# Performance work log

Hardware: AMD Instinct MI355X
Metric: run time of the kernel (lower is better)

Reference implementation:

```python
import jax, jax.numpy as jnp
import numpy as np

B, T, V, H = 16, 128, 32000, 768
P = H // 2
NBOW = 64
PAD = 0
EPS = 0.05     # label smoothing
TAU = 0.07
W_CE, W_AL, W_BOW, W_DIV, W_VAR = 1.0, 0.5, 0.2, 0.1, 0.05
BOW_IDS = jnp.arange(NBOW, dtype=jnp.int32) * 500  # registered buffer bow_indices_tensor


def _ln(x, g, b):
    m = jnp.mean(x, axis=-1, keepdims=True)
    v = jnp.mean((x - m) ** 2, axis=-1, keepdims=True)
    return (x - m) / jnp.sqrt(v + 1e-5) * g + b


def _l2norm(x):
    return x / jnp.maximum(jnp.linalg.norm(x, axis=-1, keepdims=True), 1e-12)


def _proj(x, g, bn, W1, b1, W2, b2):
    h = _ln(x, g, bn)
    h = jax.nn.gelu(h @ W1 + b1, approximate=False)  # torch nn.GELU default = exact
    return h @ W2 + b2


def setup_inputs() -> dict:
    key = jax.random.key(0)
    ks = jax.random.split(key, 12)
    s = 0.02
    return {
        "logits": jax.random.normal(ks[0], (B, T, V), dtype=jnp.float32),
        "labels": jax.random.randint(ks[1], (B, T), 0, V, dtype=jnp.int32),
        "attention_mask": jnp.ones((B, T), dtype=jnp.int32),
        "encoder_features": jax.random.normal(ks[2], (B, H), dtype=jnp.float32),
        "decoder_hidden": jax.random.normal(ks[3], (B, T, H), dtype=jnp.float32),
        "ln_g_e": jnp.ones((H,), jnp.float32), "ln_b_e": jnp.zeros((H,), jnp.float32),
        "W1_e": jax.random.normal(ks[4], (H, P), jnp.float32) * s, "b1_e": jnp.zeros((P,), jnp.float32),
        "W2_e": jax.random.normal(ks[5], (P, P), jnp.float32) * s, "b2_e": jnp.zeros((P,), jnp.float32),
        "ln_g_t": jnp.ones((H,), jnp.float32), "ln_b_t": jnp.zeros((H,), jnp.float32),
        "W1_t": jax.random.normal(ks[6], (H, P), jnp.float32) * s, "b1_t": jnp.zeros((P,), jnp.float32),
        "W2_t": jax.random.normal(ks[7], (P, P), jnp.float32) * s, "b2_t": jnp.zeros((P,), jnp.float32),
        "W_bow": jax.random.normal(ks[8], (H, NBOW), jnp.float32) * s, "b_bow": jnp.zeros((NBOW,), jnp.float32),
    }


def _forward(logits, labels, attention_mask, encoder_features, decoder_hidden,
             ln_g_e, ln_b_e, W1_e, b1_e, W2_e, b2_e,
             ln_g_t, ln_b_t, W1_t, b1_t, W2_t, b2_t,
             W_bow, b_bow):
    # --- label-smoothed CE over valid (non-pad, non -100) tokens ---
    valid = (labels != PAD) & (labels != -100)                      # (B,T)
    lab = jnp.clip(labels, 0, V - 1)
    lp = jax.nn.log_softmax(logits, axis=-1)                        # (B,T,V)
    lp_lab = jnp.take_along_axis(lp, lab[..., None], axis=-1)[..., 0]
    tok_loss = -((1.0 - EPS) * lp_lab + (EPS / V) * lp.sum(-1))     # smooth target = (1-eps) at label + eps/V everywhere
    vf = valid.astype(jnp.float32)
    ce = (tok_loss * vf).sum() / jnp.maximum(vf.sum(), 1.0)

    # --- contrastive alignment (InfoNCE both ways) ---
    m = attention_mask[..., None].astype(jnp.float32)               # (B,T,1)
    pooled = (decoder_hidden * m).sum(1) / jnp.maximum(m.sum(1), 1.0)
    z_e = _l2norm(_proj(encoder_features, ln_g_e, ln_b_e, W1_e, b1_e, W2_e, b2_e))
    z_t = _l2norm(_proj(pooled, ln_g_t, ln_b_t, W1_t, b1_t, W2_t, b2_t))
    sim = (z_e @ z_t.T) / TAU                                       # (B,B)
    li = -jnp.diag(jax.nn.log_softmax(sim, axis=-1)).mean()
    lj = -jnp.diag(jax.nn.log_softmax(sim.T, axis=-1)).mean()
    align = 0.5 * (li + lj)

    # --- BoW BCE: target[b,i] = any valid token of row b equals bow id i ---
    match = (lab[:, :, None] == BOW_IDS[None, None, :]) & valid[:, :, None]
    bow_t = match.any(axis=1).astype(jnp.float32)                   # (B,NBOW)
    bl = encoder_features @ W_bow + b_bow
    bce = jnp.mean(jnp.maximum(bl, 0.0) - bl * bow_t + jnp.log1p(jnp.exp(-jnp.abs(bl))))

    # --- diversity: mean |off-diagonal cosine sim| of encoder features ---
    nf = _l2norm(encoder_features)
    sm = nf @ nf.T
    off = 1.0 - jnp.eye(B, dtype=jnp.float32)
    div = (jnp.abs(sm) * off).sum() / (B * B - B)

    # --- variance: mean exp(-var_dim) (torch.var uses ddof=1) ---
    fvar = jnp.var(encoder_features, axis=0, ddof=1)
    var_l = jnp.mean(jnp.exp(-fvar))

    return W_CE * ce + W_AL * align + W_BOW * bce + W_DIV * div + W_VAR * var_l


def reference(logits, labels, attention_mask, encoder_features, decoder_hidden,
              ln_g_e, ln_b_e, W1_e, b1_e, W2_e, b2_e,
              ln_g_t, ln_b_t, W1_t, b1_t, W2_t, b2_t,
              W_bow, b_bow):
    return _forward(logits, labels, attention_mask, encoder_features, decoder_hidden,
                    ln_g_e, ln_b_e, W1_e, b1_e, W2_e, b2_e,
                    ln_g_t, ln_b_t, W1_t, b1_t, W2_t, b2_t,
                    W_bow, b_bow)
```

## Files before the change

kernel.cpp:

```cpp
#include <hip/hip_runtime.h>
#include <math.h>

#define BB 16
#define TT 128
#define VV 32000
#define HH 768
#define PP 384
#define NBOWD 64
#define EPS_LS 0.05f
#define TAUC 0.07f
#define NCE (BB * TT)
#define SMALLB 101

typedef float fvec4 __attribute__((ext_vector_type(4)));

__device__ __forceinline__ float blockReduceSum256(float v, float* sh4) {
  int tid = threadIdx.x;
#pragma unroll
  for (int m = 32; m > 0; m >>= 1) v += __shfl_xor(v, m, 64);
  if ((tid & 63) == 0) sh4[tid >> 6] = v;
  __syncthreads();
  float r = (sh4[0] + sh4[1]) + (sh4[2] + sh4[3]);
  __syncthreads();
  return r;
}

#define CONS(v, sA, sB, sxv)                                  \
  do {                                                        \
    sxv += (v.x + v.y) + (v.z + v.w);                         \
    sA += __expf(v.x) + __expf(v.y);                          \
    sB += __expf(v.z) + __expf(v.w);                          \
  } while (0)

#define NTL(p) __builtin_nontemporal_load(p)

__global__ __launch_bounds__(256) void fused_main(
    const float* __restrict__ logits, const int* __restrict__ labels, const int* __restrict__ amask,
    const float* __restrict__ enc, const float* __restrict__ dh,
    const float* __restrict__ g_e, const float* __restrict__ be_, const float* __restrict__ W1e,
    const float* __restrict__ b1e, const float* __restrict__ W2e, const float* __restrict__ b2e,
    const float* __restrict__ g_t, const float* __restrict__ bt_, const float* __restrict__ W1t,
    const float* __restrict__ b1t, const float* __restrict__ W2t, const float* __restrict__ b2t,
    const float* __restrict__ W_bow, const float* __restrict__ b_bow,
    float* __restrict__ tok, float* __restrict__ vfs,
    float* __restrict__ ze, float* __restrict__ zt,
    float* __restrict__ bowp, float* __restrict__ divp, float* __restrict__ var_p) {
  __shared__ float smem[2304];
  int tid = threadIdx.x;
  int blk = blockIdx.x;

  if (blk >= SMALLB) {
    int row = blk - SMALLB;
    const float* x = logits + (size_t)row * VV;
    const fvec4* x4 = (const fvec4*)x;
    const fvec4* xr = x4 + tid;
    float s0 = 0.f, s1 = 0.f, s2 = 0.f, s3 = 0.f;
    float sxa = 0.f, sxb = 0.f;

    fvec4 a0 = NTL(xr + 0),    a1 = NTL(xr + 256),  a2 = NTL(xr + 512),  a3 = NTL(xr + 768);
    fvec4 a4 = NTL(xr + 1024), a5 = NTL(xr + 1280), a6 = NTL(xr + 1536), a7 = NTL(xr + 1792);
    fvec4 b0 = NTL(xr + 2048), b1 = NTL(xr + 2304), b2 = NTL(xr + 2560), b3 = NTL(xr + 2816);
    fvec4 b4 = NTL(xr + 3072), b5 = NTL(xr + 3328), b6 = NTL(xr + 3584), b7 = NTL(xr + 3840);

    CONS(a0, s0, s1, sxa); CONS(a1, s2, s3, sxb);
    CONS(a2, s0, s1, sxa); CONS(a3, s2, s3, sxb);
    CONS(a4, s0, s1, sxa); CONS(a5, s2, s3, sxb);
    CONS(a6, s0, s1, sxa); CONS(a7, s2, s3, sxb);

    a0 = NTL(xr + 4096); a1 = NTL(xr + 4352); a2 = NTL(xr + 4608); a3 = NTL(xr + 4864);
    a4 = NTL(xr + 5120); a5 = NTL(xr + 5376); a6 = NTL(xr + 5632); a7 = NTL(xr + 5888);

    CONS(b0, s0, s1, sxa); CONS(b1, s2, s3, sxb);
    CONS(b2, s0, s1, sxa); CONS(b3, s2, s3, sxb);
    CONS(b4, s0, s1, sxa); CONS(b5, s2, s3, sxb);
    CONS(b6, s0, s1, sxa); CONS(b7, s2, s3, sxb);

    b0 = NTL(xr + 6144); b1 = NTL(xr + 6400); b2 = NTL(xr + 6656); b3 = NTL(xr + 6912);
    b4 = NTL(xr + 7168); b5 = NTL(xr + 7424); b6 = NTL(xr + 7680);

    CONS(a0, s0, s1, sxa); CONS(a1, s2, s3, sxb);
    CONS(a2, s0, s1, sxa); CONS(a3, s2, s3, sxb);
    CONS(a4, s0, s1, sxa); CONS(a5, s2, s3, sxb);
    CONS(a6, s0, s1, sxa); CONS(a7, s2, s3, sxb);

    if (tid < 64) {
      fvec4 t0 = NTL(x4 + 7936 + tid);
      CONS(t0, s0, s1, sxa);
    }

    CONS(b0, s0, s1, sxa); CONS(b1, s2, s3, sxb);
    CONS(b2, s0, s1, sxa); CONS(b3, s2, s3, sxb);
    CONS(b4, s0, s1, sxa); CONS(b5, s2, s3, sxb);
    CONS(b6, s0, s1, sxa);

    float s = (s0 + s1) + (s2 + s3);
    float sx = sxa + sxb;

#pragma unroll
    for (int m = 32; m > 0; m >>= 1) {
      s += __shfl_xor(s, m, 64);
      sx += __shfl_xor(sx, m, 64);
    }
    if ((tid & 63) == 0) { int wv = tid >> 6; smem[wv] = s; smem[4 + wv] = sx; }
    __syncthreads();
    if (tid == 0) {
      float S = (smem[0] + smem[1]) + (smem[2] + smem[3]);
      float SX = (smem[4] + smem[5]) + (smem[6] + smem[7]);
      float L = logf(S);
      int lab = labels[row];
      bool valid = (lab != 0) && (lab != -100);
      int lc = lab < 0 ? 0 : (lab > VV - 1 ? VV - 1 : lab);
      float xl = x[lc];
      float lp_lab = xl - L;
      float lp_sum = SX - (float)VV * L;
      float tl = -((1.f - EPS_LS) * lp_lab + (EPS_LS / (float)VV) * lp_sum);
      tok[row] = valid ? tl : 0.f;
      vfs[row] = valid ? 1.f : 0.f;
    }
    return;
  }

  int sblk = blk;

  if (sblk < 32) {
    float* xs = smem;
    float* hs = smem + 768;
    float* red = smem + 1152;
    float* mf = smem + 1408;
    float* fA = smem + 1536;
    float* fB = smem + 1920;
    bool is_t = sblk >= BB;
    int b = sblk & (BB - 1);
    const float *g, *bb_, *W1, *b1, *W2, *b2;
    float* zout;
    if (is_t) { g = g_t; bb_ = bt_; W1 = W1t; b1 = b1t; W2 = W2t; b2 = b2t; zout = zt; }
    else      { g = g_e; bb_ = be_; W1 = W1e; b1 = b1e; W2 = W2e; b2 = b2e; zout = ze; }

    if (is_t) {
      float mval = (tid < TT) ? (float)amask[b * TT + tid] : 0.f;
      if (tid < TT) mf[tid] = mval;
      float den = fmaxf(blockReduceSum256(mval, red), 1.f);
      const fvec4* dh4 = (const fvec4*)(dh + (size_t)b * TT * HH);
      if (tid < 192) {
        fvec4 aa = {0.f, 0.f, 0.f, 0.f}, ab = {0.f, 0.f, 0.f, 0.f};
#pragma unroll 8
        for (int t = 0; t < TT; t += 2) {
          aa += mf[t] * dh4[t * 192 + tid];
          ab += mf[t + 1] * dh4[(t + 1) * 192 + tid];
        }
        ((fvec4*)xs)[tid] = (aa + ab) * (1.f / den);
      }
    } else {
      if (tid < 192) ((fvec4*)xs)[tid] = ((const fvec4*)(enc + (size_t)b * HH))[tid];
    }
    __syncthreads();

    float s1 = 0.f, s2 = 0.f;
    for (int k = tid; k < HH; k += 256) { float v = xs[k]; s1 += v; s2 += v * v; }
    s1 = blockReduceSum256(s1, red);
    s2 = blockReduceSum256(s2, red);
    float mean = s1 / (float)HH;
    float var = s2 / (float)HH - mean * mean;
    float rstd = rsqrtf(var + 1e-5f);
    for (int k = tid; k < HH; k += 256) xs[k] = (xs[k] - mean) * rstd * g[k] + bb_[k];
    __syncthreads();

    {
      const fvec4* W1v = (const fvec4*)W1;
      if (tid < 192) {
        int kh = (tid >= 96) ? 1 : 0;
        int j4 = tid - 96 * kh;
        const fvec4* Wp = W1v + (size_t)(384 * kh) * 96 + j4;
        const float* xk = xs + 384 * kh;
        fvec4 aa = {0.f, 0.f, 0.f, 0.f}, ab = {0.f, 0.f, 0.f, 0.f};
#pragma unroll 8
        for (int k = 0; k < 384; k += 2) {
          aa += xk[k] * Wp[(size_t)k * 96];
          ab += xk[k + 1] * Wp[(size_t)(k + 1) * 96];
        }
        fvec4 acc = aa + ab;
        if (kh) ((fvec4*)fB)[j4] = acc; else ((fvec4*)fA)[j4] = acc;
      }
      __syncthreads();
      for (int j = tid; j < PP; j += 256) {
        float a = b1[j] + fA[j] + fB[j];
        hs[j] = 0.5f * a * (1.f + erff(a * 0.70710678118654752440f));
      }
      __syncthreads();
    }

    {
      const fvec4* W2v = (const fvec4*)W2;
      if (tid < 192) {
        int kh = (tid >= 96) ? 1 : 0;
        int j4 = tid - 96 * kh;
        const fvec4* Wp = W2v + (size_t)(192 * kh) * 96 + j4;
        const float* hk = hs + 192 * kh;
        fvec4 aa = {0.f, 0.f, 0.f, 0.f}, ab = {0.f, 0.f, 0.f, 0.f};
#pragma unroll 8
        for (int k = 0; k < 192; k += 2) {
          aa += hk[k] * Wp[(size_t)k * 96];
          ab += hk[k + 1] * Wp[(size_t)(k + 1) * 96];
        }
        fvec4 acc = aa + ab;
        if (kh) ((fvec4*)fB)[j4] = acc; else ((fvec4*)fA)[j4] = acc;
      }
      __syncthreads();
      for (int j = tid; j < PP; j += 256) xs[j] = b2[j] + fA[j] + fB[j];
      __syncthreads();
    }

    float sq = 0.f;
    for (int j = tid; j < PP; j += 256) { float v = xs[j]; sq += v * v; }
    sq = blockReduceSum256(sq, red);
    float inv = 1.f / fmaxf(sqrtf(sq), 1e-12f);
    for (int j = tid; j < PP; j += 256) zout[b * PP + j] = xs[j] * inv;
    return;
  }

  if (sblk < 96) {
    int bb = sblk - 32;
    int b = bb >> 2, kq = bb & 3;
    int iw = tid & 63, ks = tid >> 6;
    const float* er = enc + b * HH;
    int k0 = kq * 192 + ks * 48;
    float acc = 0.f;
#pragma unroll 8
    for (int k = 0; k < 48; ++k) acc += er[k0 + k] * W_bow[(k0 + k) * NBOWD + iw];
    smem[ks * 64 + iw] = acc;
    __syncthreads();
    if (tid < 64) bowp[bb * 64 + tid] = smem[tid] + smem[64 + tid] + smem[128 + tid] + smem[192 + tid];
    return;
  }

  if (sblk < 100) {
    int kq = sblk - 96;
    int i = tid >> 4, j = tid & 15;
    const float* a = enc + i * HH + kq * 192;
    const float* c = enc + j * HH + kq * 192;
    float a0 = 0.f, a1 = 0.f;
#pragma unroll 8
    for (int k = 0; k < 192; k += 2) {
      a0 += a[k] * c[k];
      a1 += a[k + 1] * c[k + 1];
    }
    divp[kq * 256 + tid] = a0 + a1;
    return;
  }

  {
    float vsum = 0.f;
    for (int d = tid; d < HH; d += 256) {
      float a1 = 0.f, a2 = 0.f;
#pragma unroll
      for (int b = 0; b < BB; b++) { float v = enc[b * HH + d]; a1 += v; a2 += v * v; }
      float mean = a1 / (float)BB;
      float vr = (a2 - (float)BB * mean * mean) / (float)(BB - 1);
      vsum += __expf(-vr);
    }
    float r = blockReduceSum256(vsum, smem);
    if (tid == 0) var_p[0] = r / (float)HH;
  }
}

__global__ __launch_bounds__(256) void finalize2(
    const float* __restrict__ tok, const float* __restrict__ vfs,
    const float* __restrict__ ze, const float* __restrict__ zt,
    const float* __restrict__ bowp, const float* __restrict__ divp, const float* __restrict__ var_p,
    const int* __restrict__ labels, const float* __restrict__ b_bow,
    float* __restrict__ out) {
  __shared__ float sh[8];
  __shared__ float smat[256];
  __shared__ float misc[40];
  __shared__ int flags[BB * NBOWD];
  int tid = threadIdx.x;

  for (int i = tid; i < BB * NBOWD; i += 256) flags[i] = 0;
  __syncthreads();
  for (int i = tid; i < BB * TT; i += 256) {
    int lab = labels[i];
    if (lab != 0 && lab != -100) {
      int lc = lab < 0 ? 0 : (lab > VV - 1 ? VV - 1 : lab);
      if (lc % 500 == 0) {
        int iw = lc / 500;
        if (iw < NBOWD) flags[(i >> 7) * NBOWD + iw] = 1;
      }
    }
  }

  float tsum = 0.f, csum = 0.f;
  for (int i = tid; i < BB * TT; i += 256) { tsum += tok[i]; csum += vfs[i]; }
  float ce_sum = blockReduceSum256(tsum, sh);
  float ce_cnt = blockReduceSum256(csum, sh);

  {
    int i = tid >> 4, j = tid & 15;
    const float* a = ze + i * PP;
    const float* c = zt + j * PP;
    float a0 = 0.f, a1 = 0.f;
#pragma unroll 8
    for (int k = 0; k < PP; k += 2) { a0 += a[k] * c[k]; a1 += a[k + 1] * c[k + 1]; }
    smat[tid] = (a0 + a1) * (1.f / TAUC);
  }
  __syncthreads();
  if (tid < 32) {
    bool isrow = tid < 16;
    int r = tid & 15;
    float mx = -1e30f;
    for (int j = 0; j < 16; j++) { float v = isrow ? smat[r * 16 + j] : smat[j * 16 + r]; mx = fmaxf(mx, v); }
    float se = 0.f;
    for (int j = 0; j < 16; j++) { float v = isrow ? smat[r * 16 + j] : smat[j * 16 + r]; se += __expf(v - mx); }
    misc[tid] = smat[r * 17] - mx - logf(se);
  }
  __syncthreads();
  float align;
  if (tid == 0) {
    float li = 0.f, lj = 0.f;
    for (int r = 0; r < 16; r++) { li += misc[r]; lj += misc[16 + r]; }
    misc[33] = 0.5f * (-(li / 16.f) - (lj / 16.f));
  }
  __syncthreads();
  align = misc[33];
  __syncthreads();

  float bsum = 0.f;
  for (int e = tid; e < BB * NBOWD; e += 256) {
    int b = e >> 6, iw = e & 63;
    float bl = b_bow[iw] + bowp[(b * 4 + 0) * 64 + iw] + bowp[(b * 4 + 1) * 64 + iw]
             + bowp[(b * 4 + 2) * 64 + iw] + bowp[(b * 4 + 3) * 64 + iw];
    float tgt = (float)flags[e];
    bsum += fmaxf(bl, 0.f) - bl * tgt + log1pf(__expf(-fabsf(bl)));
  }
  float bce = blockReduceSum256(bsum, sh) / (float)(BB * NBOWD);

  smat[tid] = divp[tid] + divp[256 + tid] + divp[512 + tid] + divp[768 + tid];
  __syncthreads();
  float contrib = 0.f;
  {
    int i = tid >> 4, j = tid & 15;
    if (i != j) {
      float ni = fmaxf(sqrtf(smat[i * 17]), 1e-12f);
      float nj = fmaxf(sqrtf(smat[j * 17]), 1e-12f);
      contrib = fabsf(smat[tid]) / (ni * nj);
    }
  }
  float divs = blockReduceSum256(contrib, sh) / (float)(BB * BB - BB);

  if (tid == 0) {
    float ce = ce_sum / fmaxf(ce_cnt, 1.f);
    out[0] = 1.0f * ce + 0.5f * align + 0.2f * bce + 0.1f * divs + 0.05f * var_p[0];
  }
}

extern "C" void kernel_launch(void* const* d_in, const int* in_sizes, int n_in,
                              void* d_out, int out_size, void* d_ws, size_t ws_size,
                              hipStream_t stream) {
  const float* logits = (const float*)d_in[0];
  const int* labels   = (const int*)d_in[1];
  const int* amask    = (const int*)d_in[2];
  const float* enc    = (const float*)d_in[3];
  const float* dh     = (const float*)d_in[4];
  const float* g_e    = (const float*)d_in[5];
  const float* be_    = (const float*)d_in[6];
  const float* W1e    = (const float*)d_in[7];
  const float* b1e    = (const float*)d_in[8];
  const float* W2e    = (const float*)d_in[9];
  const float* b2e    = (const float*)d_in[10];
  const float* g_t    = (const float*)d_in[11];
  const float* bt_    = (const float*)d_in[12];
  const float* W1t    = (const float*)d_in[13];
  const float* b1t    = (const float*)d_in[14];
  const float* W2t    = (const float*)d_in[15];
  const float* b2t    = (const float*)d_in[16];
  const float* W_bow  = (const float*)d_in[17];
  const float* b_bow  = (const float*)d_in[18];

  float* f     = (float*)d_ws;
  float* tok   = f;
  float* vfs   = f + 2048;
  float* ze    = f + 4096;
  float* zt    = f + 10240;
  float* bowp  = f + 16384;
  float* divp  = f + 20480;
  float* var_p = f + 21504;

  fused_main<<<SMALLB + NCE, 256, 0, stream>>>(
      logits, labels, amask, enc, dh,
      g_e, be_, W1e, b1e, W2e, b2e,
      g_t, bt_, W1t, b1t, W2t, b2t,
      W_bow, b_bow, tok, vfs, ze, zt, bowp, divp, var_p);
  finalize2<<<1, 256, 0, stream>>>(tok, vfs, ze, zt, bowp, divp, var_p, labels, b_bow, (float*)d_out);
}
```

Before: 413.7 us.

## Split projection MLPs into batched kernels and parallelize decoder pooling

Before, 32 blocks each ran a full LayerNorm+MLP for a single sample, so every block re-read W1 and W2. Those blocks now only do masked mean pooling of decoder_hidden, spread over 96 blocks. The MLP moves into two separate kernels (mlp1, mlp2), each using 48 blocks over 16-column slices, which computes all 16 rows per block so weights are read once. L2 normalization is folded into finalize2. The cost is two extra kernel launches and serialization after the large CE pass, since the MLP can no longer overlap with the logits streaming.

```diff
diff --git a/kernel.cpp b/kernel.cpp
--- a/kernel.cpp
+++ b/kernel.cpp
@@ -10,7 +10,7 @@
 #define EPS_LS 0.05f
 #define TAUC 0.07f
 #define NCE (BB * TT)
-#define SMALLB 101
+#define SMALL1 165
 
 typedef float fvec4 __attribute__((ext_vector_type(4)));
 
@@ -34,23 +34,19 @@
 
 #define NTL(p) __builtin_nontemporal_load(p)
 
-__global__ __launch_bounds__(256) void fused_main(
+__global__ __launch_bounds__(256) void ce_pool(
     const float* __restrict__ logits, const int* __restrict__ labels, const int* __restrict__ amask,
     const float* __restrict__ enc, const float* __restrict__ dh,
-    const float* __restrict__ g_e, const float* __restrict__ be_, const float* __restrict__ W1e,
-    const float* __restrict__ b1e, const float* __restrict__ W2e, const float* __restrict__ b2e,
-    const float* __restrict__ g_t, const float* __restrict__ bt_, const float* __restrict__ W1t,
-    const float* __restrict__ b1t, const float* __restrict__ W2t, const float* __restrict__ b2t,
-    const float* __restrict__ W_bow, const float* __restrict__ b_bow,
+    const float* __restrict__ W_bow,
     float* __restrict__ tok, float* __restrict__ vfs,
-    float* __restrict__ ze, float* __restrict__ zt,
+    float* __restrict__ pooled,
     float* __restrict__ bowp, float* __restrict__ divp, float* __restrict__ var_p) {
-  __shared__ float smem[2304];
+  __shared__ float smem[1280];
   int tid = threadIdx.x;
   int blk = blockIdx.x;
 
-  if (blk >= SMALLB) {
-    int row = blk - SMALLB;
+  if (blk >= SMALL1) {
+    int row = blk - SMALL1;
     const float* x = logits + (size_t)row * VV;
     const fvec4* x4 = (const fvec4*)x;
     const fvec4* xr = x4 + tid;
@@ -120,106 +116,35 @@
     return;
   }
 
-  int sblk = blk;
-
-  if (sblk < 32) {
-    float* xs = smem;
-    float* hs = smem + 768;
-    float* red = smem + 1152;
-    float* mf = smem + 1408;
-    float* fA = smem + 1536;
-    float* fB = smem + 1920;
-    bool is_t = sblk >= BB;
-    int b = sblk & (BB - 1);
-    const float *g, *bb_, *W1, *b1, *W2, *b2;
-    float* zout;
-    if (is_t) { g = g_t; bb_ = bt_; W1 = W1t; b1 = b1t; W2 = W2t; b2 = b2t; zout = zt; }
-    else      { g = g_e; bb_ = be_; W1 = W1e; b1 = b1e; W2 = W2e; b2 = b2e; zout = ze; }
-
-    if (is_t) {
-      float mval = (tid < TT) ? (float)amask[b * TT + tid] : 0.f;
-      if (tid < TT) mf[tid] = mval;
-      float den = fmaxf(blockReduceSum256(mval, red), 1.f);
-      const fvec4* dh4 = (const fvec4*)(dh + (size_t)b * TT * HH);
-      if (tid < 192) {
-        fvec4 aa = {0.f, 0.f, 0.f, 0.f}, ab = {0.f, 0.f, 0.f, 0.f};
-#pragma unroll 8
-        for (int t = 0; t < TT; t += 2) {
-          aa += mf[t] * dh4[t * 192 + tid];
-          ab += mf[t + 1] * dh4[(t + 1) * 192 + tid];
-        }
-        ((fvec4*)xs)[tid] = (aa + ab) * (1.f / den);
-      }
-    } else {
-      if (tid < 192) ((fvec4*)xs)[tid] = ((const fvec4*)(enc + (size_t)b * HH))[tid];
-    }
+  if (blk < 96) {
+    float* mf = smem;
+    float* red = smem + 128;
+    fvec4* part = (fvec4*)(smem + 136);
+    int b = blk / 6, c = blk % 6;
+    float mval = (tid < TT) ? (float)amask[b * TT + tid] : 0.f;
+    if (tid < TT) mf[tid] = mval;
+    float den = fmaxf(blockReduceSum256(mval, red), 1.f);
+    int col = tid & 31, tg = tid >> 5;
+    const fvec4* dh4 = (const fvec4*)dh + (size_t)b * TT * 192 + c * 32 + col;
+    fvec4 acc = {0.f, 0.f, 0.f, 0.f};
+#pragma unroll 8
+    for (int i = 0; i < 16; ++i) {
+      int t = tg * 16 + i;
+      acc += mf[t] * dh4[(size_t)t * 192];
+    }
+    part[tg * 32 + col] = acc;
     __syncthreads();
-
-    float s1 = 0.f, s2 = 0.f;
-    for (int k = tid; k < HH; k += 256) { float v = xs[k]; s1 += v; s2 += v * v; }
-    s1 = blockReduceSum256(s1, red);
-    s2 = blockReduceSum256(s2, red);
-    float mean = s1 / (float)HH;
-    float var = s2 / (float)HH - mean * mean;
-    float rstd = rsqrtf(var + 1e-5f);
-    for (int k = tid; k < HH; k += 256) xs[k] = (xs[k] - mean) * rstd * g[k] + bb_[k];
-    __syncthreads();
-
-    {
-      const fvec4* W1v = (const fvec4*)W1;
-      if (tid < 192) {
-        int kh = (tid >= 96) ? 1 : 0;
-        int j4 = tid - 96 * kh;
-        const fvec4* Wp = W1v + (size_t)(384 * kh) * 96 + j4;
-        const float* xk = xs + 384 * kh;
-        fvec4 aa = {0.f, 0.f, 0.f, 0.f}, ab = {0.f, 0.f, 0.f, 0.f};
-#pragma unroll 8
-        for (int k = 0; k < 384; k += 2) {
-          aa += xk[k] * Wp[(size_t)k * 96];
-          ab += xk[k + 1] * Wp[(size_t)(k + 1) * 96];
-        }
-        fvec4 acc = aa + ab;
-        if (kh) ((fvec4*)fB)[j4] = acc; else ((fvec4*)fA)[j4] = acc;
-      }
-      __syncthreads();
-      for (int j = tid; j < PP; j += 256) {
-        float a = b1[j] + fA[j] + fB[j];
-        hs[j] = 0.5f * a * (1.f + erff(a * 0.70710678118654752440f));
-      }
-      __syncthreads();
-    }
-
-    {
-      const fvec4* W2v = (const fvec4*)W2;
-      if (tid < 192) {
-        int kh = (tid >= 96) ? 1 : 0;
-        int j4 = tid - 96 * kh;
-        const fvec4* Wp = W2v + (size_t)(192 * kh) * 96 + j4;
-        const float* hk = hs + 192 * kh;
-        fvec4 aa = {0.f, 0.f, 0.f, 0.f}, ab = {0.f, 0.f, 0.f, 0.f};
-#pragma unroll 8
-        for (int k = 0; k < 192; k += 2) {
-          aa += hk[k] * Wp[(size_t)k * 96];
-          ab += hk[k + 1] * Wp[(size_t)(k + 1) * 96];
-        }
-        fvec4 acc = aa + ab;
-        if (kh) ((fvec4*)fB)[j4] = acc; else ((fvec4*)fA)[j4] = acc;
-      }
-      __syncthreads();
-      for (int j = tid; j < PP; j += 256) xs[j] = b2[j] + fA[j] + fB[j];
-      __syncthreads();
-    }
-
-    float sq = 0.f;
-    for (int j = tid; j < PP; j += 256) { float v = xs[j]; sq += v * v; }
-    sq = blockReduceSum256(sq, red);
-    float inv = 1.f / fmaxf(sqrtf(sq), 1e-12f);
-    for (int j = tid; j < PP; j += 256) zout[b * PP + j] = xs[j] * inv;
+    if (tid < 32) {
+      fvec4 s = part[tid];
+#pragma unroll
+      for (int g2 = 1; g2 < 8; ++g2) s += part[g2 * 32 + tid];
+      ((fvec4*)pooled)[b * 192 + c * 32 + tid] = s * (1.f / den);
+    }
     return;
   }
 
-  if (sblk < 96) {
-    int bb = sblk - 32;
+  if (blk < 160) {
+    int bb = blk - 96;
     int b = bb >> 2, kq = bb & 3;
     int iw = tid & 63, ks = tid >> 6;
     const float* er = enc + b * HH;
@@ -233,8 +158,8 @@
     return;
   }
 
-  if (sblk < 100) {
-    int kq = sblk - 96;
+  if (blk < 164) {
+    int kq = blk - 160;
     int i = tid >> 4, j = tid & 15;
     const float* a = enc + i * HH + kq * 192;
     const float* c = enc + j * HH + kq * 192;
@@ -263,15 +188,100 @@
   }
 }
 
+__global__ __launch_bounds__(256) void mlp1(
+    const float* __restrict__ enc, const float* __restrict__ pooled,
+    const float* __restrict__ g_e, const float* __restrict__ be_, const float* __restrict__ W1e,
+    const float* __restrict__ b1e,
+    const float* __restrict__ g_t, const float* __restrict__ bt_, const float* __restrict__ W1t,
+    const float* __restrict__ b1t,
+    float* __restrict__ hmid) {
+  __shared__ float xsl[16 * 768];
+  int tid = threadIdx.x;
+  int side = blockIdx.x / 24, jc = blockIdx.x % 24;
+  int j0 = jc * 16;
+  const float* X = side ? pooled : enc;
+  const float* g = side ? g_t : g_e;
+  const float* bb_ = side ? bt_ : be_;
+  const float* W1 = side ? W1t : W1e;
+  const float* b1 = side ? b1t : b1e;
+
+  {
+    const fvec4* X4 = (const fvec4*)X;
+    fvec4* xs4 = (fvec4*)xsl;
+#pragma unroll
+    for (int i = 0; i < 12; ++i) xs4[tid + i * 256] = X4[tid + i * 256];
+  }
+  __syncthreads();
+
+  int r = tid >> 4, l = tid & 15;
+  float s1 = 0.f, s2 = 0.f;
+  for (int k = l; k < HH; k += 16) { float v = xsl[r * HH + k]; s1 += v; s2 += v * v; }
+#pragma unroll
+  for (int m = 8; m > 0; m >>= 1) { s1 += __shfl_xor(s1, m, 16); s2 += __shfl_xor(s2, m, 16); }
+  float mean = s1 / (float)HH;
+  float var = s2 / (float)HH - mean * mean;
+  float rstd = rsqrtf(var + 1e-5f);
+  for (int k = l; k < HH; k += 16) {
+    xsl[r * HH + k] = (xsl[r * HH + k] - mean) * rstd * g[k] + bb_[k];
+  }
+  __syncthreads();
+
+  int j = j0 + l;
+  const float* Wj = W1 + j;
+  const float* xr = xsl + r * HH;
+  float a0 = 0.f, a1 = 0.f;
+#pragma unroll 8
+  for (int k = 0; k < HH; k += 2) {
+    a0 += xr[k] * Wj[(size_t)k * PP];
+    a1 += xr[k + 1] * Wj[(size_t)(k + 1) * PP];
+  }
+  float acc = b1[j] + a0 + a1;
+  hmid[(side * 16 + r) * PP + j] = 0.5f * acc * (1.f + erff(acc * 0.70710678118654752440f));
+}
+
+__global__ __launch_bounds__(256) void mlp2(
+    const float* __restrict__ hmid,
+    const float* __restrict__ W2e, const float* __restrict__ b2e,
+    const float* __restrict__ W2t, const float* __restrict__ b2t,
+    float* __restrict__ zraw) {
+  __shared__ float hsl[16 * 384];
+  int tid = threadIdx.x;
+  int side = blockIdx.x / 24, jc = blockIdx.x % 24;
+  int j0 = jc * 16;
+  const float* W2 = side ? W2t : W2e;
+  const float* b2 = side ? b2t : b2e;
+
+  {
+    const fvec4* H4 = (const fvec4*)(hmid + side * 16 * PP);
+    fvec4* hs4 = (fvec4*)hsl;
+#pragma unroll
+    for (int i = 0; i < 6; ++i) hs4[tid + i * 256] = H4[tid + i * 256];
+  }
+  __syncthreads();
+
+  int r = tid >> 4, l = tid & 15;
+  int j = j0 + l;
+  const float* Wj = W2 + j;
+  const float* hr = hsl + r * PP;
+  float a0 = 0.f, a1 = 0.f;
+#pragma unroll 8
+  for (int k = 0; k < PP; k += 2) {
+    a0 += hr[k] * Wj[(size_t)k * PP];
+    a1 += hr[k + 1] * Wj[(size_t)(k + 1) * PP];
+  }
+  zraw[(side * 16 + r) * PP + j] = b2[j] + a0 + a1;
+}
+
 __global__ __launch_bounds__(256) void finalize2(
     const float* __restrict__ tok, const float* __restrict__ vfs,
-    const float* __restrict__ ze, const float* __restrict__ zt,
+    const float* __restrict__ zraw,
     const float* __restrict__ bowp, const float* __restrict__ divp, const float* __restrict__ var_p,
     const int* __restrict__ labels, const float* __restrict__ b_bow,
     float* __restrict__ out) {
   __shared__ float sh[8];
   __shared__ float smat[256];
   __shared__ float misc[40];
+  __shared__ float nrm[32];
   __shared__ int flags[BB * NBOWD];
   int tid = threadIdx.x;
 
@@ -294,13 +304,23 @@
   float ce_cnt = blockReduceSum256(csum, sh);
 
   {
+    int r = tid >> 3, l = tid & 7;
+    float sq = 0.f;
+    for (int k = l; k < PP; k += 8) { float v = zraw[r * PP + k]; sq += v * v; }
+#pragma unroll
+    for (int m = 4; m > 0; m >>= 1) sq += __shfl_xor(sq, m, 8);
+    if (l == 0) nrm[r] = fmaxf(sqrtf(sq), 1e-12f);
+  }
+  __syncthreads();
+
+  {
     int i = tid >> 4, j = tid & 15;
-    const float* a = ze + i * PP;
-    const float* c = zt + j * PP;
+    const float* a = zraw + i * PP;
+    const float* c = zraw + (16 + j) * PP;
     float a0 = 0.f, a1 = 0.f;
 #pragma unroll 8
     for (int k = 0; k < PP; k += 2) { a0 += a[k] * c[k]; a1 += a[k + 1] * c[k + 1]; }
-    smat[tid] = (a0 + a1) * (1.f / TAUC);
+    smat[tid] = (a0 + a1) / (nrm[i] * nrm[16 + j] * TAUC);
   }
   __syncthreads();
   if (tid < 32) {
@@ -375,19 +395,20 @@
   const float* W_bow  = (const float*)d_in[17];
   const float* b_bow  = (const float*)d_in[18];
 
-  float* f     = (float*)d_ws;
-  float* tok   = f;
-  float* vfs   = f + 2048;
-  float* ze    = f + 4096;
-  float* zt    = f + 10240;
-  float* bowp  = f + 16384;
-  float* divp  = f + 20480;
-  float* var_p = f + 21504;
-
-  fused_main<<<SMALLB + NCE, 256, 0, stream>>>(
-      logits, labels, amask, enc, dh,
-      g_e, be_, W1e, b1e, W2e, b2e,
-      g_t, bt_, W1t, b1t, W2t, b2t,
-      W_bow, b_bow, tok, vfs, ze, zt, bowp, divp, var_p);
-  finalize2<<<1, 256, 0, stream>>>(tok, vfs, ze, zt, bowp, divp, var_p, labels, b_bow, (float*)d_out);
-}
+  float* f      = (float*)d_ws;
+  float* tok    = f;
+  float* vfs    = f + 2048;
+  float* pooled = f + 4096;
+  float* hmid   = f + 16384;
+  float* zraw   = f + 28672;
+  float* bowp   = f + 40960;
+  float* divp   = f + 45056;
+  float* var_p  = f + 46080;
+
+  ce_pool<<<SMALL1 + NCE, 256, 0, stream>>>(
+      logits, labels, amask, enc, dh, W_bow,
+      tok, vfs, pooled, bowp, divp, var_p);
+  mlp1<<<48, 256, 0, stream>>>(enc, pooled, g_e, be_, W1e, b1e, g_t, bt_, W1t, b1t, hmid);
+  mlp2<<<48, 256, 0, stream>>>(hmid, W2e, b2e, W2t, b2t, zraw);
+  finalize2<<<1, 256, 0, stream>>>(tok, vfs, zraw, bowp, divp, var_p, labels, b_bow, (float*)d_out);
+}
```

Result: slower. 437.9 us (+5.9%).
